# Performance work log

Hardware: AMD Instinct MI355X
Metric: run time of the kernel (lower is better)

The kernel has to match this reference:

```python
import jax, jax.numpy as jnp
import numpy as np

B, M, D, E, K = 4096, 4, 1024, 8, 2
H = 4 * D  # expert hidden dim (input_dim * 4)


def setup_inputs() -> dict:
    key = jax.random.key(0)
    k0, k1, k2, k3 = jax.random.split(key, 4)
    x = jax.random.normal(k0, (B, M, D), jnp.float32)
    Wg = jax.random.normal(k1, (D, E), jnp.float32) * (D ** -0.5)
    bg = jnp.zeros((E,), jnp.float32)
    W1 = jax.random.normal(k2, (E, D, H), jnp.float32) * (D ** -0.5)
    b1 = jnp.zeros((E, H), jnp.float32)
    W2 = jax.random.normal(k3, (E, H, D), jnp.float32) * (H ** -0.5)
    b2 = jnp.zeros((E, D), jnp.float32)
    return {"x": x, "Wg": Wg, "bg": bg, "W1": W1, "b1": b1, "W2": W2, "b2": b2}


def reference(x, Wg, bg, W1, b1, W2, b2):
    Bn, Mn, Dn = x.shape
    xf = x.reshape(-1, Dn)                      # [N, D], N = B*M
    logits = xf @ Wg + bg                       # [N, E] gating scores (eval: no noise)
    topv, topi = jax.lax.top_k(logits, K)       # [N, K]
    topw = jax.nn.softmax(topv, axis=-1)        # softmax over top-k only
    # scatter top-k weights into dense [N, E] gate matrix (zeros elsewhere)
    gates = jnp.sum(jax.nn.one_hot(topi, E, dtype=xf.dtype) * topw[..., None], axis=1)

    def body(acc, p):
        W1e, b1e, W2e, b2e, ge = p
        # Expert MLP: Linear -> exact GELU (torch nn.GELU default) -> Linear
        y = jax.nn.gelu(xf @ W1e + b1e, approximate=False) @ W2e + b2e
        return acc + ge[:, None] * y, None

    out, _ = jax.lax.scan(body, jnp.zeros_like(xf), (W1, b1, W2, b2, gates.T))
    return out.reshape(Bn, Mn, Dn)
```

## Files before the change

### kernel.cpp

```cpp
#include <hip/hip_runtime.h>
#include <hip/hip_bf16.h>
#include <cstdint>
#include <cstddef>

#define NTOK 16384
#define DIM 1024
#define NEXP 8
#define HDIM 4096
#define BM 256
#define BN 256
#define BK 64
#define MAXTILES 160
#define GRIDX_COMB 160
#define GRIDX_FALL 80
#define GEMM_SMEM 131072

typedef unsigned short u16;
typedef short bf16x8 __attribute__((ext_vector_type(8)));
typedef float f32x4 __attribute__((ext_vector_type(4)));

typedef const __attribute__((address_space(1))) void* gas_ptr;
typedef __attribute__((address_space(3))) void* las_ptr;

__device__ __forceinline__ void gload16(const void* g, void* l) {
  __builtin_amdgcn_global_load_lds((gas_ptr)g, (las_ptr)l, 16, 0, 0);
}

__device__ __forceinline__ u16 f2b(float f) {
  union { float f; unsigned u; } v;
  v.f = f;
  unsigned r = v.u + 0x7fffu + ((v.u >> 16) & 1u);
  return (u16)(r >> 16);
}

__device__ __forceinline__ float gelu_fast(float x) {
  float x2 = x * x;
  float u = x * fmaf(0.044715f, x2, 1.0f);
  float m = fminf(1.5957691216f * u, 55.0f);
  float e = __expf(m);
  float r = __builtin_amdgcn_rcpf(e + 1.0f);
  return x * e * r;
}

__device__ __forceinline__ int2 swz_block() {
  int GX = gridDim.x;
  int nwg = GX * (int)gridDim.y;
  int bid = (int)blockIdx.y * GX + (int)blockIdx.x;
  int q = nwg >> 3, r = nwg & 7;
  int xcd = bid & 7, idx = bid >> 3;
  int wg = (xcd < r) ? (xcd * (q + 1) + idx)
                     : (r * (q + 1) + (xcd - r) * q + idx);
  return make_int2(wg % GX, wg / GX);
}

__global__ __launch_bounds__(256) void gating_kernel(
    const float* __restrict__ x, const float* __restrict__ Wg,
    const float* __restrict__ bg, int* __restrict__ e01,
    float2* __restrict__ w01, int* __restrict__ counts, u16* __restrict__ xb)
{
  __shared__ float4 wgl[NEXP][256];
  __shared__ int lcnt[16];
  int t = threadIdx.x;
  if (t < 16) lcnt[t] = 0;
  float* wglf = (float*)wgl;
  const float4* wg4 = (const float4*)Wg;
  for (int i = t; i < 2048; i += 256) {
    float4 v = wg4[i];
    int d = i >> 1, eb = (i & 1) * 4;
    wglf[(eb + 0) * 1024 + d] = v.x;
    wglf[(eb + 1) * 1024 + d] = v.y;
    wglf[(eb + 2) * 1024 + d] = v.z;
    wglf[(eb + 3) * 1024 + d] = v.w;
  }
  __syncthreads();
  int lane = t & 63, wid = t >> 6;
  int tok0 = blockIdx.x * 16 + wid * 4;
  for (int s = 0; s < 4; ++s) {
    int n = tok0 + s;
    const float4* xr = (const float4*)(x + (size_t)n * DIM);
    float4 xv[4];
    #pragma unroll
    for (int k = 0; k < 4; ++k) xv[k] = xr[lane + k * 64];
    ushort4* xo = (ushort4*)(xb + (size_t)n * DIM);
    #pragma unroll
    for (int k = 0; k < 4; ++k) {
      ushort4 o;
      o.x = f2b(xv[k].x); o.y = f2b(xv[k].y); o.z = f2b(xv[k].z); o.w = f2b(xv[k].w);
      xo[lane + k * 64] = o;
    }
    double acc[NEXP];
    #pragma unroll
    for (int e = 0; e < NEXP; ++e) acc[e] = 0.0;
    #pragma unroll
    for (int k = 0; k < 4; ++k) {
      #pragma unroll
      for (int e = 0; e < NEXP; ++e) {
        float4 w = wgl[e][lane + k * 64];
        acc[e] += (double)(xv[k].x * w.x) + (double)(xv[k].y * w.y)
                + (double)(xv[k].z * w.z) + (double)(xv[k].w * w.w);
      }
    }
    #pragma unroll
    for (int e = 0; e < NEXP; ++e) {
      for (int off = 32; off; off >>= 1) acc[e] += __shfl_down(acc[e], off, 64);
    }
    if (lane == 0) {
      float v[NEXP];
      #pragma unroll
      for (int e = 0; e < NEXP; ++e) v[e] = (float)acc[e] + bg[e];
      int e0 = 0; float v0 = v[0];
      #pragma unroll
      for (int e = 1; e < NEXP; ++e) if (v[e] > v0) { v0 = v[e]; e0 = e; }
      int e1 = -1; float v1 = -1e30f;
      #pragma unroll
      for (int e = 0; e < NEXP; ++e) if (e != e0 && v[e] > v1) { v1 = v[e]; e1 = e; }
      float d = expf(v1 - v0);
      float w0 = 1.0f / (1.0f + d);
      float w1 = d * w0;
      e01[n] = e0 | (e1 << 8);
      w01[n] = make_float2(w0, w1);
      atomicAdd(&lcnt[e0], 1);
      atomicAdd(&lcnt[8 + e1], 1);
    }
  }
  __syncthreads();
  if (t < 16 && lcnt[t]) atomicAdd(&counts[t], lcnt[t]);
}

__global__ void plan_kernel(const int* __restrict__ counts, int* __restrict__ offsets,
                            int* __restrict__ cursors, int* __restrict__ numTiles,
                            int4* __restrict__ tiledir, int combined)
{
  if (threadIdx.x == 0 && blockIdx.x == 0) {
    for (int p = 0; p < 2; ++p) {
      int o = 0;
      for (int e = 0; e < NEXP; ++e) {
        offsets[p * 8 + e] = o;
        cursors[p * 8 + e] = o;
        o += counts[p * 8 + e];
      }
    }
    if (combined) {
      int idx = 0;
      for (int s = 0; s < 16; ++s) {
        int p = s >> 3, e = s & 7;
        int c = counts[s];
        int base = p * NTOK + offsets[s];
        for (int st = 0; st < c; st += BM) {
          tiledir[idx] = make_int4(e, base + st, (c - st) < BM ? (c - st) : BM, 0);
          ++idx;
        }
      }
      numTiles[0] = idx;
      numTiles[1] = 0;
    } else {
      for (int p = 0; p < 2; ++p) {
        int idx = 0;
        for (int e = 0; e < NEXP; ++e) {
          int c = counts[p * 8 + e];
          int base = p * NTOK + offsets[p * 8 + e];
          for (int st = 0; st < c; st += BM) {
            tiledir[p * MAXTILES + idx] = make_int4(e, base + st, (c - st) < BM ? (c - st) : BM, 0);
            ++idx;
          }
        }
        numTiles[p] = idx;
      }
    }
  }
}

__global__ __launch_bounds__(256) void scatter_kernel(
    const int* __restrict__ e01, const float2* __restrict__ w01,
    int* __restrict__ cursors, int* __restrict__ rowlist, float* __restrict__ roww)
{
  int n = blockIdx.x * 256 + threadIdx.x;
  int ee = e01[n];
  float2 w = w01[n];
  int e0 = ee & 255, e1 = ee >> 8;
  int p0 = atomicAdd(&cursors[e0], 1);
  rowlist[p0] = n; roww[p0] = w.x;
  int p1 = atomicAdd(&cursors[8 + e1], 1);
  rowlist[NTOK + p1] = n; roww[NTOK + p1] = w.y;
}

__global__ __launch_bounds__(256) void transpose_convert_kernel(
    const float* __restrict__ in, u16* __restrict__ out, int R, int C)
{
  __shared__ float tile[64][65];
  size_t base = (size_t)blockIdx.z * R * C;
  int r0 = blockIdx.x * 64, c0 = blockIdx.y * 64;
  int t = threadIdx.x;
  int lr = t >> 4, lc4 = (t & 15) * 4;
  #pragma unroll
  for (int i = 0; i < 4; ++i) {
    float4 v = *reinterpret_cast<const float4*>(
        &in[base + (size_t)(r0 + i * 16 + lr) * C + c0 + lc4]);
    tile[i * 16 + lr][lc4 + 0] = v.x;
    tile[i * 16 + lr][lc4 + 1] = v.y;
    tile[i * 16 + lr][lc4 + 2] = v.z;
    tile[i * 16 + lr][lc4 + 3] = v.w;
  }
  __syncthreads();
  #pragma unroll
  for (int i = 0; i < 4; ++i) {
    int oc = i * 16 + lr;
    ushort4 o;
    o.x = f2b(tile[lc4 + 0][oc]);
    o.y = f2b(tile[lc4 + 1][oc]);
    o.z = f2b(tile[lc4 + 2][oc]);
    o.w = f2b(tile[lc4 + 3][oc]);
    *reinterpret_cast<ushort4*>(&out[base + (size_t)(c0 + oc) * R + r0 + lc4]) = o;
  }
}


__global__ __launch_bounds__(512, 2) void gemm1_kernel(
    const u16* __restrict__ xb, const u16* __restrict__ w1t,
    const float* __restrict__ b1, u16* __restrict__ h,
    const int* __restrict__ rowlist, const int4* __restrict__ tiledir,
    const int* __restrict__ numTiles, int hbase)
{
  extern __shared__ u16 smem[];
  u16* Aldsb = smem;
  u16* Bldsb = smem + 32768;
  __shared__ int tok[BM];
  int2 bxy = swz_block();
  int bx = bxy.x, by = bxy.y;
  if (bx >= *numTiles) return;
  int4 td = tiledir[bx];
  int e = td.x, row0 = td.y, rows = td.z;
  int n0 = by * BN;
  int t = threadIdx.x, lane = t & 63, wid = t >> 6;
  for (int i = t; i < BM; i += 512) {
    int p = row0 + i; if (p > 2 * NTOK - 1) p = 2 * NTOK - 1;
    tok[i] = rowlist[p];
  }
  __syncthreads();
  int schunk = (lane & 7) ^ (lane >> 3);
  const u16* gA[4]; const u16* gB[4];
  #pragma unroll
  for (int i = 0; i < 4; ++i) {
    int row = (wid * 4 + i) * 8 + (lane >> 3);
    gA[i] = xb + (size_t)tok[row] * DIM + schunk * 8;
    gB[i] = w1t + ((size_t)e * HDIM + n0 + row) * DIM + schunk * 8;
  }
  f32x4 acc[8][4] = {};
  int wr = wid >> 2, wc = wid & 3;
  int arow = lane & 15, cbase = lane >> 4, csw = arow & 7;
  #pragma unroll
  for (int i = 0; i < 4; ++i) {
    gload16(gA[i], &Aldsb[(wid * 4 + i) * 512]);
    gload16(gB[i], &Bldsb[(wid * 4 + i) * 512]);
  }
  __syncthreads();
  const int NKT = DIM / BK;
  for (int kt = 0; kt < NKT; ++kt) {
    int buf = kt & 1;
    if (kt + 1 < NKT) {
      int bo = (buf ^ 1) * 16384;
      #pragma unroll
      for (int i = 0; i < 4; ++i) {
        gload16(gA[i] + (kt + 1) * BK, &Aldsb[bo + (wid * 4 + i) * 512]);
        gload16(gB[i] + (kt + 1) * BK, &Bldsb[bo + (wid * 4 + i) * 512]);
      }
    }
    const u16* Ab = Aldsb + buf * 16384;
    const u16* Bb = Bldsb + buf * 16384;
    #pragma unroll
    for (int kk = 0; kk < 2; ++kk) {
      int cp = ((kk * 4 + cbase) ^ csw) * 8;
      bf16x8 a[8], b[4];
      #pragma unroll
      for (int m = 0; m < 8; ++m)
        a[m] = *reinterpret_cast<const bf16x8*>(&Ab[(wr * 128 + m * 16 + arow) * BK + cp]);
      #pragma unroll
      for (int n = 0; n < 4; ++n)
        b[n] = *reinterpret_cast<const bf16x8*>(&Bb[(wc * 64 + n * 16 + arow) * BK + cp]);
      __builtin_amdgcn_s_setprio(1);
      #pragma unroll
      for (int m = 0; m < 8; ++m)
        #pragma unroll
        for (int n = 0; n < 4; ++n)
          acc[m][n] = __builtin_amdgcn_mfma_f32_16x16x32_bf16(a[m], b[n], acc[m][n], 0, 0, 0);
      __builtin_amdgcn_s_setprio(0);
    }
    __syncthreads();
  }
  int rsub = (lane >> 4) * 4;
  #pragma unroll
  for (int m = 0; m < 8; ++m) {
    int lrb = wr * 128 + m * 16 + rsub;
    #pragma unroll
    for (int n = 0; n < 4; ++n) {
      int col = n0 + wc * 64 + n * 16 + arow;
      float bv = b1[e * HDIM + col];
      #pragma unroll
      for (int r = 0; r < 4; ++r) {
        int lr = lrb + r;
        if (lr < rows) {
          float v = gelu_fast(acc[m][n][r] + bv);
          h[(size_t)(row0 + lr - hbase) * HDIM + col] = f2b(v);
        }
      }
    }
  }
}

__global__ __launch_bounds__(512, 2) void gemm2_kernel(
    const u16* __restrict__ h, const u16* __restrict__ w2t,
    const float* __restrict__ b2, float* __restrict__ out,
    const int* __restrict__ rowlist, const float* __restrict__ roww,
    const int4* __restrict__ tiledir, const int* __restrict__ numTiles, int hbase)
{
  extern __shared__ u16 smem[];
  u16* Aldsb = smem;
  u16* Bldsb = smem + 32768;
  __shared__ int tok[BM];
  __shared__ float wt[BM];
  int2 bxy = swz_block();
  int bx = bxy.x, by = bxy.y;
  if (bx >= *numTiles) return;
  int4 td = tiledir[bx];
  int e = td.x, row0 = td.y, rows = td.z;
  int n0 = by * BN;
  int t = threadIdx.x, lane = t & 63, wid = t >> 6;
  for (int i = t; i < BM; i += 512) {
    int p = row0 + i; if (p > 2 * NTOK - 1) p = 2 * NTOK - 1;
    tok[i] = rowlist[p];
    wt[i] = roww[p];
  }
  __syncthreads();
  int schunk = (lane & 7) ^ (lane >> 3);
  const u16* gA[4]; const u16* gB[4];
  #pragma unroll
  for (int i = 0; i < 4; ++i) {
    int row = (wid * 4 + i) * 8 + (lane >> 3);
    int hr = row < rows ? row : (rows - 1);
    gA[i] = h + (size_t)(row0 + hr - hbase) * HDIM + schunk * 8;
    gB[i] = w2t + ((size_t)e * DIM + n0 + row) * HDIM + schunk * 8;
  }
  f32x4 acc[8][4] = {};
  int wr = wid >> 2, wc = wid & 3;
  int arow = lane & 15, cbase = lane >> 4, csw = arow & 7;
  #pragma unroll
  for (int i = 0; i < 4; ++i) {
    gload16(gA[i], &Aldsb[(wid * 4 + i) * 512]);
    gload16(gB[i], &Bldsb[(wid * 4 + i) * 512]);
  }
  __syncthreads();
  const int NKT = HDIM / BK;
  for (int kt = 0; kt < NKT; ++kt) {
    int buf = kt & 1;
    if (kt + 1 < NKT) {
      int bo = (buf ^ 1) * 16384;
      #pragma unroll
      for (int i = 0; i < 4; ++i) {
        gload16(gA[i] + (kt + 1) * BK, &Aldsb[bo + (wid * 4 + i) * 512]);
        gload16(gB[i] + (kt + 1) * BK, &Bldsb[bo + (wid * 4 + i) * 512]);
      }
    }
    const u16* Ab = Aldsb + buf * 16384;
    const u16* Bb = Bldsb + buf * 16384;
    #pragma unroll
    for (int kk = 0; kk < 2; ++kk) {
      int cp = ((kk * 4 + cbase) ^ csw) * 8;
      bf16x8 a[8], b[4];
      #pragma unroll
      for (int m = 0; m < 8; ++m)
        a[m] = *reinterpret_cast<const bf16x8*>(&Ab[(wr * 128 + m * 16 + arow) * BK + cp]);
      #pragma unroll
      for (int n = 0; n < 4; ++n)
        b[n] = *reinterpret_cast<const bf16x8*>(&Bb[(wc * 64 + n * 16 + arow) * BK + cp]);
      __builtin_amdgcn_s_setprio(1);
      #pragma unroll
      for (int m = 0; m < 8; ++m)
        #pragma unroll
        for (int n = 0; n < 4; ++n)
          acc[m][n] = __builtin_amdgcn_mfma_f32_16x16x32_bf16(a[m], b[n], acc[m][n], 0, 0, 0);
      __builtin_amdgcn_s_setprio(0);
    }
    __syncthreads();
  }
  int rsub = (lane >> 4) * 4;
  #pragma unroll
  for (int m = 0; m < 8; ++m) {
    int lrb = wr * 128 + m * 16 + rsub;
    #pragma unroll
    for (int n = 0; n < 4; ++n) {
      int col = n0 + wc * 64 + n * 16 + arow;
      float bv = b2[e * DIM + col];
      #pragma unroll
      for (int r = 0; r < 4; ++r) {
        int lr = lrb + r;
        if (lr < rows) {
          float v = (acc[m][n][r] + bv) * wt[lr];
          atomicAdd(&out[(size_t)tok[lr] * DIM + col], v);
        }
      }
    }
  }
}

extern "C" void kernel_launch(void* const* d_in, const int* in_sizes, int n_in,
                              void* d_out, int out_size, void* d_ws, size_t ws_size,
                              hipStream_t stream)
{
  const float* x  = (const float*)d_in[0];
  const float* Wg = (const float*)d_in[1];
  const float* bg = (const float*)d_in[2];
  const float* W1 = (const float*)d_in[3];
  const float* b1 = (const float*)d_in[4];
  const float* W2 = (const float*)d_in[5];
  const float* b2 = (const float*)d_in[6];
  float* out = (float*)d_out;

  const size_t SZ_XB  = (size_t)NTOK * DIM * 2;
  const size_t SZ_W1T = (size_t)NEXP * DIM * HDIM * 2;
  const size_t SZ_W2T = (size_t)NEXP * HDIM * DIM * 2;
  const size_t SZ_H1  = (size_t)NTOK * HDIM * 2;
  const size_t SZ_TAIL = (size_t)2 * NTOK * 4 + (size_t)2 * NTOK * 4
                       + (size_t)NTOK * 4 + (size_t)NTOK * 8 + 256
                       + (size_t)2 * MAXTILES * 16 + 1024;
  const size_t NEED_COMB = SZ_XB + SZ_W1T + SZ_W2T + 2 * SZ_H1 + SZ_TAIL;
  int combined = (ws_size >= NEED_COMB) ? 1 : 0;
  size_t szh = combined ? 2 * SZ_H1 : SZ_H1;

  char* ws = (char*)d_ws;
  const size_t OFF_XB  = 0;
  const size_t OFF_W1T = OFF_XB  + SZ_XB;
  const size_t OFF_W2T = OFF_W1T + SZ_W1T;
  const size_t OFF_H   = OFF_W2T + SZ_W2T;
  const size_t OFF_RL  = OFF_H   + szh;
  const size_t OFF_RW  = OFF_RL  + (size_t)2 * NTOK * 4;
  const size_t OFF_E01 = OFF_RW  + (size_t)2 * NTOK * 4;
  const size_t OFF_W01 = OFF_E01 + (size_t)NTOK * 4;
  const size_t OFF_META= OFF_W01 + (size_t)NTOK * 8;
  const size_t OFF_DIR = OFF_META + 256;

  u16*    xb      = (u16*)(ws + OFF_XB);
  u16*    w1t     = (u16*)(ws + OFF_W1T);
  u16*    w2t     = (u16*)(ws + OFF_W2T);
  u16*    h       = (u16*)(ws + OFF_H);
  int*    rowlist = (int*)(ws + OFF_RL);
  float*  roww    = (float*)(ws + OFF_RW);
  int*    e01     = (int*)(ws + OFF_E01);
  float2* w01     = (float2*)(ws + OFF_W01);
  int*    meta    = (int*)(ws + OFF_META);
  int*    counts   = meta;
  int*    offsets  = meta + 16;
  int*    cursors  = meta + 32;
  int*    numTiles = meta + 48;
  int4*   tiledir  = (int4*)(ws + OFF_DIR);

  hipMemsetAsync(meta, 0, 256, stream);
  hipMemsetAsync(out, 0, (size_t)out_size * 4, stream);

  gating_kernel<<<NTOK / 16, 256, 0, stream>>>(x, Wg, bg, e01, w01, counts, xb);
  plan_kernel<<<1, 64, 0, stream>>>(counts, offsets, cursors, numTiles, tiledir, combined);
  scatter_kernel<<<NTOK / 256, 256, 0, stream>>>(e01, w01, cursors, rowlist, roww);

  transpose_convert_kernel<<<dim3(DIM / 64, HDIM / 64, NEXP), 256, 0, stream>>>(W1, w1t, DIM, HDIM);
  transpose_convert_kernel<<<dim3(HDIM / 64, DIM / 64, NEXP), 256, 0, stream>>>(W2, w2t, HDIM, DIM);

  if (combined) {
    gemm1_kernel<<<dim3(GRIDX_COMB, HDIM / BN), 512, GEMM_SMEM, stream>>>(
        xb, w1t, b1, h, rowlist, tiledir, numTiles, 0);
    gemm2_kernel<<<dim3(GRIDX_COMB, DIM / BN), 512, GEMM_SMEM, stream>>>(
        h, w2t, b2, out, rowlist, roww, tiledir, numTiles, 0);
  } else {
    gemm1_kernel<<<dim3(GRIDX_FALL, HDIM / BN), 512, GEMM_SMEM, stream>>>(
        xb, w1t, b1, h, rowlist, tiledir, numTiles, 0);
    gemm2_kernel<<<dim3(GRIDX_FALL, DIM / BN), 512, GEMM_SMEM, stream>>>(
        h, w2t, b2, out, rowlist, roww, tiledir, numTiles, 0);
    gemm1_kernel<<<dim3(GRIDX_FALL, HDIM / BN), 512, GEMM_SMEM, stream>>>(
        xb, w1t, b1, h, rowlist, tiledir + MAXTILES, numTiles + 1, NTOK);
    gemm2_kernel<<<dim3(GRIDX_FALL, DIM / BN), 512, GEMM_SMEM, stream>>>(
        h, w2t, b2, out, rowlist, roww, tiledir + MAXTILES, numTiles + 1, NTOK);
  }
}
```

Measured before the change: 1.129 ms.

## Shrink expert GEMM tiles to 128x128 with single-buffered LDS and higher occupancy

Both expert GEMM kernels move from 256x256 tiles with 8 waves and double-buffered 128KB LDS to 128x128 tiles with 4 waves and a single 32KB LDS buffer. Launch bounds change to allow 3 blocks per CU, and the grid and tile-directory sizes grow to match the smaller tiles. The intent is better CU load balance on the uneven per-expert row counts, and latency hiding through more resident blocks rather than in-block prefetch. In exchange, data reuse per tile halves, so global and LDS traffic per FLOP rises. Each k-step now waits on its own loads, with no overlap inside a block.

```diff
diff --git a/kernel.cpp b/kernel.cpp
--- a/kernel.cpp
+++ b/kernel.cpp
@@ -7,13 +7,13 @@
 #define DIM 1024
 #define NEXP 8
 #define HDIM 4096
-#define BM 256
-#define BN 256
+#define BM 128
+#define BN 128
 #define BK 64
-#define MAXTILES 160
-#define GRIDX_COMB 160
-#define GRIDX_FALL 80
-#define GEMM_SMEM 131072
+#define MAXTILES 384
+#define GRIDX_COMB 272
+#define GRIDX_FALL 144
+#define GEMM_SMEM 32768
 
 typedef unsigned short u16;
 typedef short bf16x8 __attribute__((ext_vector_type(8)));
@@ -215,15 +215,13 @@
 }
 
 
-__global__ __launch_bounds__(512, 2) void gemm1_kernel(
+__global__ __launch_bounds__(256, 3) void gemm1_kernel(
     const u16* __restrict__ xb, const u16* __restrict__ w1t,
     const float* __restrict__ b1, u16* __restrict__ h,
     const int* __restrict__ rowlist, const int4* __restrict__ tiledir,
     const int* __restrict__ numTiles, int hbase)
 {
   extern __shared__ u16 smem[];
-  u16* Aldsb = smem;
-  u16* Bldsb = smem + 32768;
   __shared__ int tok[BM];
   int2 bxy = swz_block();
   int bx = bxy.x, by = bxy.y;
@@ -232,54 +230,44 @@
   int e = td.x, row0 = td.y, rows = td.z;
   int n0 = by * BN;
   int t = threadIdx.x, lane = t & 63, wid = t >> 6;
-  for (int i = t; i < BM; i += 512) {
+  for (int i = t; i < BM; i += 256) {
     int p = row0 + i; if (p > 2 * NTOK - 1) p = 2 * NTOK - 1;
     tok[i] = rowlist[p];
   }
   __syncthreads();
-  int schunk = (lane & 7) ^ (lane >> 3);
-  const u16* gA[4]; const u16* gB[4];
+  int qoff[4]; const u16* gA[4]; const u16* gB[4];
   #pragma unroll
   for (int i = 0; i < 4; ++i) {
-    int row = (wid * 4 + i) * 8 + (lane >> 3);
-    gA[i] = xb + (size_t)tok[row] * DIM + schunk * 8;
-    gB[i] = w1t + ((size_t)e * HDIM + n0 + row) * DIM + schunk * 8;
-  }
-  f32x4 acc[8][4] = {};
-  int wr = wid >> 2, wc = wid & 3;
+    int q = t + i * 256;
+    int row = q >> 3, c = (q & 7) ^ (row & 7);
+    qoff[i] = q * 8;
+    gA[i] = xb + (size_t)tok[row] * DIM + c * 8;
+    gB[i] = w1t + ((size_t)e * HDIM + n0 + row) * DIM + c * 8;
+  }
+  f32x4 acc[4][4] = {};
+  int wr = wid >> 1, wc = wid & 1;
   int arow = lane & 15, cbase = lane >> 4, csw = arow & 7;
-  #pragma unroll
-  for (int i = 0; i < 4; ++i) {
-    gload16(gA[i], &Aldsb[(wid * 4 + i) * 512]);
-    gload16(gB[i], &Bldsb[(wid * 4 + i) * 512]);
-  }
-  __syncthreads();
   const int NKT = DIM / BK;
   for (int kt = 0; kt < NKT; ++kt) {
-    int buf = kt & 1;
-    if (kt + 1 < NKT) {
-      int bo = (buf ^ 1) * 16384;
-      #pragma unroll
-      for (int i = 0; i < 4; ++i) {
-        gload16(gA[i] + (kt + 1) * BK, &Aldsb[bo + (wid * 4 + i) * 512]);
-        gload16(gB[i] + (kt + 1) * BK, &Bldsb[bo + (wid * 4 + i) * 512]);
-      }
-    }
-    const u16* Ab = Aldsb + buf * 16384;
-    const u16* Bb = Bldsb + buf * 16384;
+    #pragma unroll
+    for (int i = 0; i < 4; ++i) {
+      gload16(gA[i] + kt * BK, &smem[qoff[i]]);
+      gload16(gB[i] + kt * BK, &smem[8192 + qoff[i]]);
+    }
+    __syncthreads();
     #pragma unroll
     for (int kk = 0; kk < 2; ++kk) {
       int cp = ((kk * 4 + cbase) ^ csw) * 8;
-      bf16x8 a[8], b[4];
-      #pragma unroll
-      for (int m = 0; m < 8; ++m)
-        a[m] = *reinterpret_cast<const bf16x8*>(&Ab[(wr * 128 + m * 16 + arow) * BK + cp]);
+      bf16x8 a[4], b[4];
+      #pragma unroll
+      for (int m = 0; m < 4; ++m)
+        a[m] = *reinterpret_cast<const bf16x8*>(&smem[(wr * 64 + m * 16 + arow) * 64 + cp]);
       #pragma unroll
       for (int n = 0; n < 4; ++n)
-        b[n] = *reinterpret_cast<const bf16x8*>(&Bb[(wc * 64 + n * 16 + arow) * BK + cp]);
+        b[n] = *reinterpret_cast<const bf16x8*>(&smem[8192 + (wc * 64 + n * 16 + arow) * 64 + cp]);
       __builtin_amdgcn_s_setprio(1);
       #pragma unroll
-      for (int m = 0; m < 8; ++m)
+      for (int m = 0; m < 4; ++m)
         #pragma unroll
         for (int n = 0; n < 4; ++n)
           acc[m][n] = __builtin_amdgcn_mfma_f32_16x16x32_bf16(a[m], b[n], acc[m][n], 0, 0, 0);
@@ -289,8 +277,8 @@
   }
   int rsub = (lane >> 4) * 4;
   #pragma unroll
-  for (int m = 0; m < 8; ++m) {
-    int lrb = wr * 128 + m * 16 + rsub;
+  for (int m = 0; m < 4; ++m) {
+    int lrb = wr * 64 + m * 16 + rsub;
     #pragma unroll
     for (int n = 0; n < 4; ++n) {
       int col = n0 + wc * 64 + n * 16 + arow;
@@ -307,15 +295,13 @@
   }
 }
 
-__global__ __launch_bounds__(512, 2) void gemm2_kernel(
+__global__ __launch_bounds__(256, 3) void gemm2_kernel(
     const u16* __restrict__ h, const u16* __restrict__ w2t,
     const float* __restrict__ b2, float* __restrict__ out,
     const int* __restrict__ rowlist, const float* __restrict__ roww,
     const int4* __restrict__ tiledir, const int* __restrict__ numTiles, int hbase)
 {
   extern __shared__ u16 smem[];
-  u16* Aldsb = smem;
-  u16* Bldsb = smem + 32768;
   __shared__ int tok[BM];
   __shared__ float wt[BM];
   int2 bxy = swz_block();
@@ -325,56 +311,46 @@
   int e = td.x, row0 = td.y, rows = td.z;
   int n0 = by * BN;
   int t = threadIdx.x, lane = t & 63, wid = t >> 6;
-  for (int i = t; i < BM; i += 512) {
+  for (int i = t; i < BM; i += 256) {
     int p = row0 + i; if (p > 2 * NTOK - 1) p = 2 * NTOK - 1;
     tok[i] = rowlist[p];
     wt[i] = roww[p];
   }
   __syncthreads();
-  int schunk = (lane & 7) ^ (lane >> 3);
-  const u16* gA[4]; const u16* gB[4];
+  int qoff[4]; const u16* gA[4]; const u16* gB[4];
   #pragma unroll
   for (int i = 0; i < 4; ++i) {
-    int row = (wid * 4 + i) * 8 + (lane >> 3);
+    int q = t + i * 256;
+    int row = q >> 3, c = (q & 7) ^ (row & 7);
+    qoff[i] = q * 8;
     int hr = row < rows ? row : (rows - 1);
-    gA[i] = h + (size_t)(row0 + hr - hbase) * HDIM + schunk * 8;
-    gB[i] = w2t + ((size_t)e * DIM + n0 + row) * HDIM + schunk * 8;
-  }
-  f32x4 acc[8][4] = {};
-  int wr = wid >> 2, wc = wid & 3;
+    gA[i] = h + (size_t)(row0 + hr - hbase) * HDIM + c * 8;
+    gB[i] = w2t + ((size_t)e * DIM + n0 + row) * HDIM + c * 8;
+  }
+  f32x4 acc[4][4] = {};
+  int wr = wid >> 1, wc = wid & 1;
   int arow = lane & 15, cbase = lane >> 4, csw = arow & 7;
-  #pragma unroll
-  for (int i = 0; i < 4; ++i) {
-    gload16(gA[i], &Aldsb[(wid * 4 + i) * 512]);
-    gload16(gB[i], &Bldsb[(wid * 4 + i) * 512]);
-  }
-  __syncthreads();
   const int NKT = HDIM / BK;
   for (int kt = 0; kt < NKT; ++kt) {
-    int buf = kt & 1;
-    if (kt + 1 < NKT) {
-      int bo = (buf ^ 1) * 16384;
-      #pragma unroll
-      for (int i = 0; i < 4; ++i) {
-        gload16(gA[i] + (kt + 1) * BK, &Aldsb[bo + (wid * 4 + i) * 512]);
-        gload16(gB[i] + (kt + 1) * BK, &Bldsb[bo + (wid * 4 + i) * 512]);
-      }
-    }
-    const u16* Ab = Aldsb + buf * 16384;
-    const u16* Bb = Bldsb + buf * 16384;
+    #pragma unroll
+    for (int i = 0; i < 4; ++i) {
+      gload16(gA[i] + kt * BK, &smem[qoff[i]]);
+      gload16(gB[i] + kt * BK, &smem[8192 + qoff[i]]);
+    }
+    __syncthreads();
     #pragma unroll
     for (int kk = 0; kk < 2; ++kk) {
       int cp = ((kk * 4 + cbase) ^ csw) * 8;
-      bf16x8 a[8], b[4];
-      #pragma unroll
-      for (int m = 0; m < 8; ++m)
-        a[m] = *reinterpret_cast<const bf16x8*>(&Ab[(wr * 128 + m * 16 + arow) * BK + cp]);
+      bf16x8 a[4], b[4];
+      #pragma unroll
+      for (int m = 0; m < 4; ++m)
+        a[m] = *reinterpret_cast<const bf16x8*>(&smem[(wr * 64 + m * 16 + arow) * 64 + cp]);
       #pragma unroll
       for (int n = 0; n < 4; ++n)
-        b[n] = *reinterpret_cast<const bf16x8*>(&Bb[(wc * 64 + n * 16 + arow) * BK + cp]);
+        b[n] = *reinterpret_cast<const bf16x8*>(&smem[8192 + (wc * 64 + n * 16 + arow) * 64 + cp]);
       __builtin_amdgcn_s_setprio(1);
       #pragma unroll
-      for (int m = 0; m < 8; ++m)
+      for (int m = 0; m < 4; ++m)
         #pragma unroll
         for (int n = 0; n < 4; ++n)
           acc[m][n] = __builtin_amdgcn_mfma_f32_16x16x32_bf16(a[m], b[n], acc[m][n], 0, 0, 0);
@@ -384,8 +360,8 @@
   }
   int rsub = (lane >> 4) * 4;
   #pragma unroll
-  for (int m = 0; m < 8; ++m) {
-    int lrb = wr * 128 + m * 16 + rsub;
+  for (int m = 0; m < 4; ++m) {
+    int lrb = wr * 64 + m * 16 + rsub;
     #pragma unroll
     for (int n = 0; n < 4; ++n) {
       int col = n0 + wc * 64 + n * 16 + arow;
@@ -464,18 +440,18 @@
   transpose_convert_kernel<<<dim3(HDIM / 64, DIM / 64, NEXP), 256, 0, stream>>>(W2, w2t, HDIM, DIM);
 
   if (combined) {
-    gemm1_kernel<<<dim3(GRIDX_COMB, HDIM / BN), 512, GEMM_SMEM, stream>>>(
+    gemm1_kernel<<<dim3(GRIDX_COMB, HDIM / BN), 256, GEMM_SMEM, stream>>>(
         xb, w1t, b1, h, rowlist, tiledir, numTiles, 0);
-    gemm2_kernel<<<dim3(GRIDX_COMB, DIM / BN), 512, GEMM_SMEM, stream>>>(
+    gemm2_kernel<<<dim3(GRIDX_COMB, DIM / BN), 256, GEMM_SMEM, stream>>>(
         h, w2t, b2, out, rowlist, roww, tiledir, numTiles, 0);
   } else {
-    gemm1_kernel<<<dim3(GRIDX_FALL, HDIM / BN), 512, GEMM_SMEM, stream>>>(
+    gemm1_kernel<<<dim3(GRIDX_FALL, HDIM / BN), 256, GEMM_SMEM, stream>>>(
         xb, w1t, b1, h, rowlist, tiledir, numTiles, 0);
-    gemm2_kernel<<<dim3(GRIDX_FALL, DIM / BN), 512, GEMM_SMEM, stream>>>(
+    gemm2_kernel<<<dim3(GRIDX_FALL, DIM / BN), 256, GEMM_SMEM, stream>>>(
         h, w2t, b2, out, rowlist, roww, tiledir, numTiles, 0);
-    gemm1_kernel<<<dim3(GRIDX_FALL, HDIM / BN), 512, GEMM_SMEM, stream>>>(
+    gemm1_kernel<<<dim3(GRIDX_FALL, HDIM / BN), 256, GEMM_SMEM, stream>>>(
         xb, w1t, b1, h, rowlist, tiledir + MAXTILES, numTiles + 1, NTOK);
-    gemm2_kernel<<<dim3(GRIDX_FALL, DIM / BN), 512, GEMM_SMEM, stream>>>(
+    gemm2_kernel<<<dim3(GRIDX_FALL, DIM / BN), 256, GEMM_SMEM, stream>>>(
         h, w2t, b2, out, rowlist, roww, tiledir + MAXTILES, numTiles + 1, NTOK);
   }
 }
```

After: 1.119 ms. No clear change (-1.0%).
